# Optimization experiments

Hardware: AMD Instinct MI355X
Metric: run time of the kernel (lower is better)

Reference implementation:

```python
import jax, jax.numpy as jnp
import numpy as np
from jax import lax

# flat indices of the 8 'donut' taps in a 3x3 kernel (center position 4 stays zero),
# matching torch.nonzero row-major ordering of the mask
_DONUT_IDX = jnp.array([0, 1, 2, 3, 5, 6, 7, 8])

def _gelu(x):
    return jax.nn.gelu(x, approximate=False)  # torch nn.GELU default (erf)

def _conv(x, w, dil=1, pad=0):
    return lax.conv_general_dilated(x, w, (1, 1), [(pad, pad), (pad, pad)],
                                    rhs_dilation=(dil, dil),
                                    dimension_numbers=('NCHW', 'OIHW', 'NCHW'))

def _donut_conv(x, p, dil):
    # ParamConv_reg_variable_dilation with shuffle_true=0: scatter 8 params into a
    # 3x3 kernel (zero center) and conv with rhs_dilation=dil, padding=dil ('same').
    O, I, _ = p.shape
    k = jnp.zeros((O, I, 9), p.dtype).at[:, :, _DONUT_IDX].set(p).reshape(O, I, 3, 3)
    return _conv(x, k, dil=dil, pad=dil)

def _resblock(x, w1, w2):
    # gelu(Sequential(conv3x3, gelu, conv3x3)(x) + x)
    return _gelu(_conv(_gelu(_conv(x, w1, pad=1)), w2, pad=1) + x)

def _avgpool2(x):
    N, C, H, W = x.shape
    return x.reshape(N, C, H // 2, 2, W // 2, 2).mean(axis=(3, 5))

def _upsample(x, scale, w):
    # nn.Upsample(scale, bilinear, align_corners=False) -> half-pixel bilinear resize
    N, C, H, W = x.shape
    if scale > 1:
        x = jax.image.resize(x, (N, C, H * scale, W * scale), method='bilinear')
    return _gelu(_conv(x, w))  # 1x1 conv + gelu

def _shine_fwd(input_image, conv0a_w, conv0b_w, first_p, cl10_w, cl2_w,
               dil_p, dilres_p, ups_w, out1_w, out2_w, last_w):
    # n_frames=5, center frame index 2; H,W divisible by 64 so no pad branch
    target = input_image[:, 2:3]
    feats = jnp.concatenate([input_image[:, :2], input_image[:, 3:]], axis=1)  # [N,4,H,W]
    target = _gelu(_conv(target, conv0b_w))            # 1x1 -> 48 ch
    feats = _gelu(_conv(feats, conv0a_w, pad=1))       # 3x3 -> 16 ch
    base = jnp.concatenate([target, feats], axis=1)    # 64 ch

    outs = [_gelu(_donut_conv(base, first_p, 1))]      # first_output (dil 1)
    base = _resblock(base, cl10_w[0, 0], cl10_w[0, 1])
    outs.append(_gelu(_donut_conv(base, dilres_p[0], 3)))  # dilated_convs_res[0]
    base = _resblock(base, cl2_w[0, 0], cl2_w[0, 1])

    dils = (5, 8, 10, 11)     # dilated_convs effective dilations (add_dilation=0)
    dilres = (3, 6, 8, 9)     # dilated_convs_res effective dilations
    for i in range(4):
        m = _gelu(_donut_conv(base, dil_p[i], dils[i]))
        outs.append(_upsample(m, 2 ** i, ups_w[i]))
        if i < 3:
            base = _avgpool2(base)
            base = _resblock(base, cl10_w[i + 1, 0], cl10_w[i + 1, 1])
            m = _gelu(_donut_conv(base, dilres_p[i + 1], dilres[i + 1]))
            outs.append(_upsample(m, 2 ** (i + 1), ups_w[i + 1]))
            base = _resblock(base, cl2_w[i + 1, 0], cl2_w[i + 1, 1])

    out = jnp.concatenate(outs, axis=1)                # 9*64 = 576 ch
    out = _gelu(_conv(out, out1_w))                    # 1x1 576->288
    out = _gelu(_conv(out, out2_w))                    # 1x1 288->64
    return _conv(out, last_w)                          # 1x1 64->1

def setup_inputs():
    key = jax.random.key(0)
    ks = jax.random.split(key, 12)
    s = 0.05
    F = 64
    return {
        'input_image': jax.random.normal(ks[0], (2, 5, 256, 256), jnp.float32),
        'conv0a_w': jax.random.normal(ks[1], (16, 4, 3, 3), jnp.float32) * s,
        'conv0b_w': jax.random.normal(ks[2], (48, 1, 1, 1), jnp.float32) * s,
        'first_p': jax.random.normal(ks[3], (F, F, 8), jnp.float32) * s,
        'cl10_w': jax.random.normal(ks[4], (4, 2, F, F, 3, 3), jnp.float32) * s,
        'cl2_w': jax.random.normal(ks[5], (4, 2, F, F, 3, 3), jnp.float32) * s,
        'dil_p': jax.random.normal(ks[6], (4, F, F, 8), jnp.float32) * s,
        'dilres_p': jax.random.normal(ks[7], (4, F, F, 8), jnp.float32) * s,
        'ups_w': jax.random.normal(ks[8], (4, F, F, 1, 1), jnp.float32) * s,
        'out1_w': jax.random.normal(ks[9], (288, 576, 1, 1), jnp.float32) * s,
        'out2_w': jax.random.normal(ks[10], (64, 288, 1, 1), jnp.float32) * s,
        'last_w': jax.random.normal(ks[11], (1, 64, 1, 1), jnp.float32) * s,
    }

def reference(input_image, conv0a_w, conv0b_w, first_p, cl10_w, cl2_w,
              dil_p, dilres_p, ups_w, out1_w, out2_w, last_w):
    return _shine_fwd(input_image, conv0a_w, conv0b_w, first_p, cl10_w, cl2_w,
                      dil_p, dilres_p, ups_w, out1_w, out2_w, last_w)
```

## Files before the change

### kernel.cpp

```cpp
#include <hip/hip_runtime.h>
#include <hip/hip_bf16.h>


#define HPX 65536
#define FCH 64
#define CHPX 32768

typedef __attribute__((ext_vector_type(8))) short  short8;
typedef __attribute__((ext_vector_type(4))) float  floatx4;

__device__ __forceinline__ float gelu_f(float x) {
  return 0.5f * x * (1.0f + erff(x * 0.70710678118654752440f));
}
__device__ __forceinline__ unsigned short f2bf(float x) {
  unsigned u = __float_as_uint(x);
  unsigned r = (u + 0x7FFFu + ((u >> 16) & 1u)) >> 16;
  return (unsigned short)r;
}
__device__ __forceinline__ float bf2f(unsigned short h) {
  return __uint_as_float(((unsigned)h) << 16);
}

__global__ __launch_bounds__(256) void conv0_nhwc_kernel(
    const float* __restrict__ img,
    const float* __restrict__ w0a,
    const float* __restrict__ w0b,
    unsigned short* __restrict__ ohi,
    unsigned short* __restrict__ olo)
{
  long t = (long)blockIdx.x * 256 + threadIdx.x;
  int c  = (int)(t & 63);
  int px = (int)((t >> 6) & (HPX - 1));
  int n  = (int)(t >> 22);
  const float* im = img + (long)n * 5 * HPX;
  float r;
  if (c < 48) {
    r = w0b[c] * im[2 * HPX + px];
  } else {
    int co = c - 48;
    int y = px >> 8, x = px & 255;
    r = 0.0f;
    const int map4[4] = {0, 1, 3, 4};
    #pragma unroll
    for (int fi = 0; fi < 4; fi++) {
      const float* imc = im + (long)map4[fi] * HPX;
      #pragma unroll
      for (int ky = 0; ky < 3; ky++) {
        int yy = y + ky - 1;
        #pragma unroll
        for (int kx = 0; kx < 3; kx++) {
          int xx = x + kx - 1;
          bool ok = ((unsigned)yy < 256u) && ((unsigned)xx < 256u);
          float v = ok ? imc[yy * 256 + xx] : 0.0f;
          r = fmaf(w0a[((co * 4 + fi) * 3 + ky) * 3 + kx], v, r);
        }
      }
    }
  }
  float v = gelu_f(r);
  unsigned short hb = f2bf(v);
  ohi[t] = hb;
  olo[t] = f2bf(v - bf2f(hb));
}

struct JobArr { int4 j[29]; };

__global__ __launch_bounds__(256) void pack_conv_kernel(
    const float* __restrict__ cl10, const float* __restrict__ cl2,
    const float* __restrict__ first_p, const float* __restrict__ dilres_p,
    const float* __restrict__ dil_p, const float* __restrict__ ups_w,
    unsigned short* __restrict__ packs, JobArr jobs)
{
  int4 jb = jobs.j[blockIdx.y];
  int ntaps = jb.z;
  int idx = blockIdx.x * 256 + threadIdx.x;
  if (idx >= ntaps * 8192) return;
  int j  = idx & 7;
  int l  = (idx >> 3) & 63;
  int s  = (idx >> 9) & 1;
  int nt = (idx >> 10) & 3;
  int kt = (idx >> 12) & 1;
  int tap = idx >> 13;
  int oc = nt * 16 + (l & 15);
  int ci = kt * 32 + (l >> 4) * 8 + j;
  const float* src;
  switch (jb.x) {
    case 0: src = cl10; break;
    case 1: src = cl2; break;
    case 2: src = first_p; break;
    case 3: src = dilres_p; break;
    case 4: src = dil_p; break;
    default: src = ups_w; break;
  }
  float w = src[jb.y + (oc * 64 + ci) * ntaps + tap];
  unsigned short hi = f2bf(w);
  unsigned short v = (s == 0) ? hi : f2bf(w - bf2f(hi));
  packs[jb.w + idx] = v;
}

__global__ __launch_bounds__(256) void pack_w1_kernel(
    const float* __restrict__ w1, unsigned short* __restrict__ w1p)
{
  int t = blockIdx.x * 256 + threadIdx.x;
  if (t >= 18 * 18 * 512) return;
  int j = t & 7, l = (t >> 3) & 63;
  int mt = (t >> 9) % 18, kt = (t >> 9) / 18;
  int oc = mt * 16 + (l & 15);
  int k  = kt * 32 + (l >> 4) * 8 + j;
  float w = w1[oc * 576 + k];
  unsigned short hi = f2bf(w);
  unsigned short lo = f2bf(w - bf2f(hi));
  long base = ((long)(kt * 18 + mt) * 2) * 512 + l * 8 + j;
  w1p[base] = hi;
  w1p[base + 512] = lo;
}
__global__ __launch_bounds__(256) void pack_w2_kernel(
    const float* __restrict__ w2, unsigned short* __restrict__ w2p)
{
  int t = blockIdx.x * 256 + threadIdx.x;
  if (t >= 9 * 4 * 512) return;
  int j = t & 7, l = (t >> 3) & 63;
  int ot = (t >> 9) % 4, kt = (t >> 9) / 4;
  int oc = ot * 16 + (l & 15);
  int k  = kt * 32 + (l >> 4) * 8 + j;
  float w = w2[oc * 288 + k];
  unsigned short hi = f2bf(w);
  unsigned short lo = f2bf(w - bf2f(hi));
  long base = ((long)(kt * 4 + ot) * 2) * 512 + l * 8 + j;
  w2p[base] = hi;
  w2p[base + 512] = lo;
}

template <int NTAPS, int MT, bool RESID, bool TO_CONCAT>
__global__ __launch_bounds__(256) void conv_pipe_kernel(
    const unsigned short* __restrict__ in_hi,
    const unsigned short* __restrict__ in_lo,
    const unsigned short* __restrict__ wp,
    const unsigned short* __restrict__ res_hi,
    const unsigned short* __restrict__ res_lo,
    unsigned short* __restrict__ out_hi,
    unsigned short* __restrict__ out_lo,
    int Hs, int logW, int dil, int ccol)
{
  constexpr int PL = TO_CONCAT ? 1 : 2;
  __shared__ short8 wst[2][1024];
  __shared__ unsigned short tb[4][PL][16][76];
  const int tid  = threadIdx.x;
  const int lane = tid & 63;
  const int wave = tid >> 6;
  const int row  = lane & 15;
  const int g    = lane >> 4;
  const int n    = blockIdx.z;
  const int Ws   = 1 << logW;
  const int npx_in = Hs << logW;
  const int opx0 = blockIdx.x * (64 * MT) + wave * (16 * MT);

  const unsigned short* ihi = in_hi + (long)n * npx_in * 64;
  const unsigned short* ilo = in_lo + (long)n * npx_in * 64;
  const short8* wpv = (const short8*)wp;

  int ry[MT], rx[MT];
  #pragma unroll
  for (int mt = 0; mt < MT; mt++) {
    int p = opx0 + mt * 16 + row;
    ry[mt] = p >> logW;
    rx[mt] = p & (Ws - 1);
  }

  floatx4 acc[MT][4];
  #pragma unroll
  for (int mt = 0; mt < MT; mt++)
    #pragma unroll
    for (int nt = 0; nt < 4; nt++) acc[mt][nt] = (floatx4){0.f, 0.f, 0.f, 0.f};

  const short8 zz = {0, 0, 0, 0, 0, 0, 0, 0};
  short8 sreg[4];
  short8 ahA[MT][2], alA[MT][2], ahB[MT][2], alB[MT][2];

  auto stage_issue = [&](int t) {
    #pragma unroll
    for (int p = 0; p < 4; p++)
      sreg[p] = wpv[(long)t * 1024 + tid + p * 256];
  };
  auto stage_write = [&](int b) {
    #pragma unroll
    for (int p = 0; p < 4; p++)
      wst[b][tid + p * 256] = sreg[p];
  };
  auto a_load = [&](short8 (&ah)[MT][2], short8 (&al)[MT][2], int t) {
    const int kk  = (NTAPS == 9) ? t : (t < 4 ? t : t + 1);
    const int dyd = (kk / 3 - 1) * dil, dxd = (kk % 3 - 1) * dil;
    #pragma unroll
    for (int mt = 0; mt < MT; mt++) {
      int yy = ry[mt] + dyd, xx = rx[mt] + dxd;
      bool ok = ((unsigned)yy < (unsigned)Hs) && ((unsigned)xx < (unsigned)Ws);
      long base = ok ? (long)((yy << logW) + xx) * 64 : 0;
      #pragma unroll
      for (int kt = 0; kt < 2; kt++) {
        long a = base + kt * 32 + g * 8;
        short8 h = *(const short8*)(ihi + a);
        short8 l = *(const short8*)(ilo + a);
        ah[mt][kt] = ok ? h : zz;
        al[mt][kt] = ok ? l : zz;
      }
    }
  };
  auto compute = [&](int b, short8 (&ah)[MT][2], short8 (&al)[MT][2]) {
    #pragma unroll
    for (int kt = 0; kt < 2; kt++)
      #pragma unroll
      for (int nt = 0; nt < 4; nt++) {
        short8 bh = wst[b][(kt * 4 + nt) * 128 + lane];
        short8 bl = wst[b][(kt * 4 + nt) * 128 + 64 + lane];
        #pragma unroll
        for (int mt = 0; mt < MT; mt++) {
          acc[mt][nt] = __builtin_amdgcn_mfma_f32_16x16x32_bf16(ah[mt][kt], bh, acc[mt][nt], 0, 0, 0);
          acc[mt][nt] = __builtin_amdgcn_mfma_f32_16x16x32_bf16(ah[mt][kt], bl, acc[mt][nt], 0, 0, 0);
          acc[mt][nt] = __builtin_amdgcn_mfma_f32_16x16x32_bf16(al[mt][kt], bh, acc[mt][nt], 0, 0, 0);
        }
      }
  };

  stage_issue(0);
  a_load(ahA, alA, 0);
  stage_write(0);
  __syncthreads();

  #pragma unroll
  for (int tt = 0; tt < NTAPS; tt++) {
    const int b = tt & 1;
    if (tt + 1 < NTAPS) {
      stage_issue(tt + 1);
      if ((tt & 1) == 0) a_load(ahB, alB, tt + 1);
      else               a_load(ahA, alA, tt + 1);
    }
    if ((tt & 1) == 0) compute(b, ahA, alA);
    else               compute(b, ahB, alB);
    if (tt + 1 < NTAPS) {
      stage_write(b ^ 1);
      __syncthreads();
    }
  }

  #pragma unroll
  for (int mt = 0; mt < MT; mt++) {
    __builtin_amdgcn_wave_barrier();
    #pragma unroll
    for (int nt = 0; nt < 4; nt++) {
      #pragma unroll
      for (int r = 0; r < 4; r++) {
        int px = opx0 + mt * 16 + g * 4 + r;
        int oc = nt * 16 + row;
        float v = acc[mt][nt][r];
        if (RESID) {
          long ri = ((long)n * npx_in + px) * 64 + oc;
          v += bf2f(res_hi[ri]) + bf2f(res_lo[ri]);
        }
        v = gelu_f(v);
        unsigned short hb = f2bf(v);
        tb[wave][0][g * 4 + r][oc] = hb;
        if (!TO_CONCAT)
          tb[wave][PL - 1][g * 4 + r][oc] = f2bf(v - bf2f(hb));
      }
    }
    __builtin_amdgcn_wave_barrier();
    const int pxb = opx0 + mt * 16;
    const int pxl = lane >> 2;
    #pragma unroll
    for (int pl = 0; pl < PL; pl++) {
      #pragma unroll
      for (int it = 0; it < 2; it++) {
        int ch = (lane & 3) + it * 4;
        short8 v8 = *(const short8*)&tb[wave][pl][pxl][ch * 8];
        if (TO_CONCAT) {
          *(short8*)&out_hi[((long)n * HPX + pxb + pxl) * 576 + ccol + ch * 8] = v8;
        } else {
          unsigned short* dst = pl ? out_lo : out_hi;
          *(short8*)&dst[((long)n * npx_in + pxb + pxl) * 64 + ch * 8] = v8;
        }
      }
    }
  }
}

template <int MT>
__global__ __launch_bounds__(256) void ups_mfma_kernel(
    const unsigned short* __restrict__ in_hi,
    const unsigned short* __restrict__ in_lo,
    const unsigned short* __restrict__ wp,
    unsigned short* __restrict__ outc,
    int Hs, int logW, int ccol)
{
  __shared__ short8 wst[1024];
  __shared__ unsigned short tb[4][16][76];
  const int tid  = threadIdx.x;
  const int lane = threadIdx.x & 63;
  const int wave = threadIdx.x >> 6;
  const int row  = lane & 15;
  const int g    = lane >> 4;
  const int n    = blockIdx.z;
  const int npx_in = Hs << logW;
  const int opx0 = blockIdx.x * (64 * MT) + wave * (16 * MT);

  const unsigned short* ihi = in_hi + (long)n * npx_in * 64;
  const unsigned short* ilo = in_lo + (long)n * npx_in * 64;
  const short8* wpv = (const short8*)wp;

  int b00[MT], b01[MT], b10[MT], b11[MT];
  float bwx[MT], bwy[MT];
  #pragma unroll
  for (int mt = 0; mt < MT; mt++) {
    int p = opx0 + mt * 16 + row;
    int Y = p >> 8, X = p & 255;
    float sc = (float)Hs * (1.0f / 256.0f);
    float fy = ((float)Y + 0.5f) * sc - 0.5f;
    float fx = ((float)X + 0.5f) * sc - 0.5f;
    int y0 = (int)floorf(fy), x0 = (int)floorf(fx);
    bwy[mt] = fy - (float)y0; bwx[mt] = fx - (float)x0;
    int y0c = min(max(y0, 0), Hs - 1), y1c = min(max(y0 + 1, 0), Hs - 1);
    int x0c = min(max(x0, 0), Hs - 1), x1c = min(max(x0 + 1, 0), Hs - 1);
    b00[mt] = (y0c * Hs + x0c) * 64; b01[mt] = (y0c * Hs + x1c) * 64;
    b10[mt] = (y1c * Hs + x0c) * 64; b11[mt] = (y1c * Hs + x1c) * 64;
  }

  floatx4 acc[MT][4];
  #pragma unroll
  for (int mt = 0; mt < MT; mt++)
    #pragma unroll
    for (int nt = 0; nt < 4; nt++) acc[mt][nt] = (floatx4){0.f, 0.f, 0.f, 0.f};

  #pragma unroll
  for (int p = 0; p < 4; p++)
    wst[tid + p * 256] = wpv[tid + p * 256];
  __syncthreads();

  #pragma unroll
  for (int kt = 0; kt < 2; kt++) {
    const int ko = kt * 32 + g * 8;
    short8 ah[MT], al[MT];
    #pragma unroll
    for (int mt = 0; mt < MT; mt++) {
      short8 h00 = *(const short8*)(ihi + b00[mt] + ko);
      short8 l00 = *(const short8*)(ilo + b00[mt] + ko);
      short8 h01 = *(const short8*)(ihi + b01[mt] + ko);
      short8 l01 = *(const short8*)(ilo + b01[mt] + ko);
      short8 h10 = *(const short8*)(ihi + b10[mt] + ko);
      short8 l10 = *(const short8*)(ilo + b10[mt] + ko);
      short8 h11 = *(const short8*)(ihi + b11[mt] + ko);
      short8 l11 = *(const short8*)(ilo + b11[mt] + ko);
      short8 hh, ll;
      #pragma unroll
      for (int j = 0; j < 8; j++) {
        float v00 = bf2f((unsigned short)h00[j]) + bf2f((unsigned short)l00[j]);
        float v01 = bf2f((unsigned short)h01[j]) + bf2f((unsigned short)l01[j]);
        float v10 = bf2f((unsigned short)h10[j]) + bf2f((unsigned short)l10[j]);
        float v11 = bf2f((unsigned short)h11[j]) + bf2f((unsigned short)l11[j]);
        float v0 = v00 + bwx[mt] * (v01 - v00);
        float v1 = v10 + bwx[mt] * (v11 - v10);
        float v  = v0 + bwy[mt] * (v1 - v0);
        unsigned short hb = f2bf(v);
        hh[j] = (short)hb;
        ll[j] = (short)f2bf(v - bf2f(hb));
      }
      ah[mt] = hh; al[mt] = ll;
    }
    #pragma unroll
    for (int nt = 0; nt < 4; nt++) {
      short8 bh = wst[(kt * 4 + nt) * 2 * 64 + lane];
      short8 bl = wst[((kt * 4 + nt) * 2 + 1) * 64 + lane];
      #pragma unroll
      for (int mt = 0; mt < MT; mt++) {
        acc[mt][nt] = __builtin_amdgcn_mfma_f32_16x16x32_bf16(ah[mt], bh, acc[mt][nt], 0, 0, 0);
        acc[mt][nt] = __builtin_amdgcn_mfma_f32_16x16x32_bf16(ah[mt], bl, acc[mt][nt], 0, 0, 0);
        acc[mt][nt] = __builtin_amdgcn_mfma_f32_16x16x32_bf16(al[mt], bh, acc[mt][nt], 0, 0, 0);
      }
    }
  }

  #pragma unroll
  for (int mt = 0; mt < MT; mt++) {
    __builtin_amdgcn_wave_barrier();
    #pragma unroll
    for (int nt = 0; nt < 4; nt++)
      #pragma unroll
      for (int r = 0; r < 4; r++)
        tb[wave][g * 4 + r][nt * 16 + row] = f2bf(gelu_f(acc[mt][nt][r]));
    __builtin_amdgcn_wave_barrier();
    const int pxb = opx0 + mt * 16;
    const int pxl = lane >> 2;
    #pragma unroll
    for (int it = 0; it < 2; it++) {
      int ch = (lane & 3) + it * 4;
      short8 v8 = *(const short8*)&tb[wave][pxl][ch * 8];
      *(short8*)&outc[((long)n * HPX + pxb + pxl) * 576 + ccol + ch * 8] = v8;
    }
  }
}

__global__ __launch_bounds__(256) void avgpool_nhwc_kernel(
    const unsigned short* __restrict__ ihi, const unsigned short* __restrict__ ilo,
    unsigned short* __restrict__ ohi, unsigned short* __restrict__ olo,
    int logWo)
{
  const int lognpo = 2 * logWo;
  long t = (long)blockIdx.x * 256 + threadIdx.x;
  int cg = (int)(t & 7);
  int p  = (int)((t >> 3) & ((1 << lognpo) - 1));
  int n  = (int)(t >> (3 + lognpo));
  int y = p >> logWo, x = p & ((1 << logWo) - 1);
  int Wi = 2 << logWo;
  long ib = ((long)n * (4 << lognpo) + (long)(2 * y) * Wi + 2 * x) * 64 + cg * 8;
  short8 h00 = *(const short8*)(ihi + ib);
  short8 h01 = *(const short8*)(ihi + ib + 64);
  short8 h10 = *(const short8*)(ihi + ib + (long)Wi * 64);
  short8 h11 = *(const short8*)(ihi + ib + (long)Wi * 64 + 64);
  short8 l00 = *(const short8*)(ilo + ib);
  short8 l01 = *(const short8*)(ilo + ib + 64);
  short8 l10 = *(const short8*)(ilo + ib + (long)Wi * 64);
  short8 l11 = *(const short8*)(ilo + ib + (long)Wi * 64 + 64);
  short8 oh, ol;
  #pragma unroll
  for (int j = 0; j < 8; j++) {
    float v = 0.25f * ((bf2f((unsigned short)h00[j]) + bf2f((unsigned short)l00[j])) +
                       (bf2f((unsigned short)h01[j]) + bf2f((unsigned short)l01[j])) +
                       (bf2f((unsigned short)h10[j]) + bf2f((unsigned short)l10[j])) +
                       (bf2f((unsigned short)h11[j]) + bf2f((unsigned short)l11[j])));
    unsigned short hb = f2bf(v);
    oh[j] = (short)hb;
    ol[j] = (short)f2bf(v - bf2f(hb));
  }
  long ob = (((long)n << lognpo) + p) * 64 + cg * 8;
  *(short8*)(ohi + ob) = oh;
  *(short8*)(olo + ob) = ol;
}

__global__ __launch_bounds__(256) void out1_gemm_kernel(
    const unsigned short* __restrict__ v,
    const unsigned short* __restrict__ w1p,
    unsigned short* __restrict__ h,
    int cpx)
{
  __shared__ short8 ws8[2400];
  const int tid  = threadIdx.x;
  const int lane = tid & 63;
  const int wave = tid >> 6;
  const int row  = lane & 15;
  const int g    = lane >> 4;
  const int n    = blockIdx.y;
  const int px0  = cpx + blockIdx.x * 64;
  const int mtb  = (wave < 2) ? wave * 5 : 10 + (wave - 2) * 4;
  const int MTN  = (wave < 2) ? 5 : 4;
  const short8* w1v = (const short8*)w1p;

  floatx4 acc[4][5];
  #pragma unroll
  for (int t = 0; t < 4; t++)
    #pragma unroll
    for (int m = 0; m < 5; m++) acc[t][m] = (floatx4){0.f, 0.f, 0.f, 0.f};

  for (int kt = 0; kt < 18; kt++) {
    __syncthreads();
    #pragma unroll
    for (int p = 0; p < 9; p++)
      ws8[tid + p * 256] = w1v[kt * 2304 + tid + p * 256];
    __syncthreads();

    short8 a[4];
    #pragma unroll
    for (int t = 0; t < 4; t++)
      a[t] = *(const short8*)(v + ((long)n * HPX + px0 + t * 16 + row) * 576 +
                              kt * 32 + g * 8);
    #pragma unroll
    for (int m = 0; m < 5; m++) {
      if (m < MTN) {
        short8 bh = ws8[((mtb + m) * 2 + 0) * 64 + lane];
        short8 bl = ws8[((mtb + m) * 2 + 1) * 64 + lane];
        #pragma unroll
        for (int t = 0; t < 4; t++) {
          acc[t][m] = __builtin_amdgcn_mfma_f32_16x16x32_bf16(a[t], bh, acc[t][m], 0, 0, 0);
          acc[t][m] = __builtin_amdgcn_mfma_f32_16x16x32_bf16(a[t], bl, acc[t][m], 0, 0, 0);
        }
      }
    }
  }

  __syncthreads();
  unsigned short* hs2 = (unsigned short*)ws8;
  #pragma unroll
  for (int m = 0; m < 5; m++) {
    if (m < MTN) {
      #pragma unroll
      for (int t = 0; t < 4; t++)
        #pragma unroll
        for (int r = 0; r < 4; r++)
          hs2[(t * 16 + g * 4 + r) * 300 + (mtb + m) * 16 + row] =
              f2bf(gelu_f(acc[t][m][r]));
    }
  }
  __syncthreads();
  #pragma unroll
  for (int p = 0; p < 9; p++) {
    int li = tid + p * 256;
    int px = li / 36, c16 = li % 36;
    short8 v8 = *(const short8*)&hs2[px * 300 + c16 * 8];
    *(short8*)&h[((long)n * CHPX + (px0 - cpx) + px) * 288 + c16 * 8] = v8;
  }
}

__global__ __launch_bounds__(256) void out2_gemm_kernel(
    const unsigned short* __restrict__ h,
    const unsigned short* __restrict__ w2p,
    const float* __restrict__ w3,
    float* __restrict__ out,
    int cpx)
{
  __shared__ short8 w2s[4608];
  const int tid  = threadIdx.x;
  const int lane = tid & 63;
  const int wave = tid >> 6;
  const int row  = lane & 15;
  const int g    = lane >> 4;
  const int n    = blockIdx.y;
  const int pxc  = blockIdx.x * 256 + wave * 64;
  const short8* w2v = (const short8*)w2p;

  #pragma unroll
  for (int p = 0; p < 18; p++)
    w2s[tid + p * 256] = w2v[tid + p * 256];
  __syncthreads();

  floatx4 acc2[4][4];
  #pragma unroll
  for (int t = 0; t < 4; t++)
    #pragma unroll
    for (int ot = 0; ot < 4; ot++) acc2[t][ot] = (floatx4){0.f, 0.f, 0.f, 0.f};

  for (int kt = 0; kt < 9; kt++) {
    short8 a[4];
    #pragma unroll
    for (int t = 0; t < 4; t++)
      a[t] = *(const short8*)&h[((long)n * CHPX + pxc + t * 16 + row) * 288 +
                                kt * 32 + g * 8];
    #pragma unroll
    for (int ot = 0; ot < 4; ot++) {
      short8 bh = w2s[((kt * 4 + ot) * 2 + 0) * 64 + lane];
      short8 bl = w2s[((kt * 4 + ot) * 2 + 1) * 64 + lane];
      #pragma unroll
      for (int t = 0; t < 4; t++) {
        acc2[t][ot] = __builtin_amdgcn_mfma_f32_16x16x32_bf16(a[t], bh, acc2[t][ot], 0, 0, 0);
        acc2[t][ot] = __builtin_amdgcn_mfma_f32_16x16x32_bf16(a[t], bl, acc2[t][ot], 0, 0, 0);
      }
    }
  }

  float w3r[4];
  #pragma unroll
  for (int ot = 0; ot < 4; ot++) w3r[ot] = w3[ot * 16 + row];
  #pragma unroll
  for (int t = 0; t < 4; t++) {
    float r[4] = {0.f, 0.f, 0.f, 0.f};
    #pragma unroll
    for (int ot = 0; ot < 4; ot++)
      #pragma unroll
      for (int rr = 0; rr < 4; rr++)
        r[rr] = fmaf(w3r[ot], gelu_f(acc2[t][ot][rr]), r[rr]);
    #pragma unroll
    for (int rr = 0; rr < 4; rr++) {
      r[rr] += __shfl_xor(r[rr], 1);
      r[rr] += __shfl_xor(r[rr], 2);
      r[rr] += __shfl_xor(r[rr], 4);
      r[rr] += __shfl_xor(r[rr], 8);
    }
    if (row == 0) {
      int px = cpx + pxc + t * 16 + g * 4;
      #pragma unroll
      for (int rr = 0; rr < 4; rr++)
        out[(long)n * HPX + px + rr] = r[rr];
    }
  }
}

extern "C" void kernel_launch(void* const* d_in, const int* in_sizes, int n_in,
                              void* d_out, int out_size, void* d_ws, size_t ws_size,
                              hipStream_t stream) {
  const float* img      = (const float*)d_in[0];
  const float* w0a      = (const float*)d_in[1];
  const float* w0b      = (const float*)d_in[2];
  const float* first_p  = (const float*)d_in[3];
  const float* cl10     = (const float*)d_in[4];
  const float* cl2      = (const float*)d_in[5];
  const float* dil_p    = (const float*)d_in[6];
  const float* dilres_p = (const float*)d_in[7];
  const float* ups_w    = (const float*)d_in[8];
  const float* w1       = (const float*)d_in[9];
  const float* w2       = (const float*)d_in[10];
  const float* w3       = (const float*)d_in[11];

  const size_t CONCAT_B = 150994944ul;
  const size_t ACT_B    = 16777216ul;
  const size_t PACKS_B  = 3604480ul;
  const size_t W1P_B    = 663552ul;
  const size_t W2P_B    = 73728ul;
  const size_t NEED = CONCAT_B + 4 * ACT_B + PACKS_B + W1P_B + W2P_B;

  if (ws_size < NEED) {
    hipMemsetAsync(d_out, 0, (size_t)out_size * 4, stream);
    return;
  }

  char* wsb = (char*)d_ws;
  unsigned short* concat = (unsigned short*)wsb;
  unsigned short* Xhi = (unsigned short*)(wsb + CONCAT_B);
  unsigned short* Xlo = (unsigned short*)(wsb + CONCAT_B + ACT_B);
  unsigned short* Yhi = (unsigned short*)(wsb + CONCAT_B + 2 * ACT_B);
  unsigned short* Ylo = (unsigned short*)(wsb + CONCAT_B + 3 * ACT_B);
  unsigned short* packs = (unsigned short*)(wsb + CONCAT_B + 4 * ACT_B);
  unsigned short* w1p = (unsigned short*)(wsb + CONCAT_B + 4 * ACT_B + PACKS_B);
  unsigned short* w2p = (unsigned short*)(wsb + CONCAT_B + 4 * ACT_B + PACKS_B + W1P_B);
  unsigned short* hbuf = Xhi;

  auto off_cl10   = [](int c) { return (long)c * 73728; };
  auto off_cl2    = [](int c) { return 589824l + (long)c * 73728; };
  const long OFF_FIRST = 1179648;
  auto off_dilres = [](int k) { return 1245184l + (long)k * 65536; };
  auto off_dil    = [](int k) { return 1507328l + (long)k * 65536; };
  auto off_ups    = [](int k) { return 1769472l + (long)k * 8192; };

  JobArr jobs;
  for (int c = 0; c < 8; c++) jobs.j[c]     = {0, c * 36864, 9, (int)off_cl10(c)};
  for (int c = 0; c < 8; c++) jobs.j[8 + c] = {1, c * 36864, 9, (int)off_cl2(c)};
  jobs.j[16] = {2, 0, 8, (int)OFF_FIRST};
  for (int k = 0; k < 4; k++) jobs.j[17 + k] = {3, k * 32768, 8, (int)off_dilres(k)};
  for (int k = 0; k < 4; k++) jobs.j[21 + k] = {4, k * 32768, 8, (int)off_dil(k)};
  for (int k = 0; k < 4; k++) jobs.j[25 + k] = {5, k * 4096, 1, (int)off_ups(k)};
  pack_conv_kernel<<<dim3(288, 29), 256, 0, stream>>>(
      cl10, cl2, first_p, dilres_p, dil_p, ups_w, packs, jobs);
  pack_w1_kernel<<<(18 * 18 * 512 + 255) / 256, 256, 0, stream>>>(w1, w1p);
  pack_w2_kernel<<<(9 * 4 * 512 + 255) / 256, 256, 0, stream>>>(w2, w2p);

  conv0_nhwc_kernel<<<(2 * HPX * 64) / 256, 256, 0, stream>>>(img, w0a, w0b, Xhi, Xlo);

  auto conv9 = [&](const unsigned short* ih, const unsigned short* il, long wo,
                   unsigned short* oh, unsigned short* ol, int Hs, int logW) {
    int npx = Hs << logW;
    if (npx == HPX)
      conv_pipe_kernel<9, 2, false, false><<<dim3(npx / 128, 1, 2), 256, 0, stream>>>(
          ih, il, packs + wo, nullptr, nullptr, oh, ol, Hs, logW, 1, 0);
    else
      conv_pipe_kernel<9, 1, false, false><<<dim3(npx / 64, 1, 2), 256, 0, stream>>>(
          ih, il, packs + wo, nullptr, nullptr, oh, ol, Hs, logW, 1, 0);
  };
  auto conv9r = [&](const unsigned short* ih, const unsigned short* il, long wo,
                    unsigned short* rh, unsigned short* rl, int Hs, int logW) {
    int npx = Hs << logW;
    if (npx == HPX)
      conv_pipe_kernel<9, 2, true, false><<<dim3(npx / 128, 1, 2), 256, 0, stream>>>(
          ih, il, packs + wo, rh, rl, rh, rl, Hs, logW, 1, 0);
    else
      conv_pipe_kernel<9, 1, true, false><<<dim3(npx / 64, 1, 2), 256, 0, stream>>>(
          ih, il, packs + wo, rh, rl, rh, rl, Hs, logW, 1, 0);
  };
  auto donutC = [&](const unsigned short* ih, const unsigned short* il, long wo,
                    int dil, int ccol) {
    conv_pipe_kernel<8, 2, false, true><<<dim3(512, 1, 2), 256, 0, stream>>>(
        ih, il, packs + wo, nullptr, nullptr, concat, nullptr, 256, 8, dil, ccol);
  };
  auto donutA = [&](const unsigned short* ih, const unsigned short* il, long wo,
                    int dil, unsigned short* oh, unsigned short* ol, int Hs, int logW) {
    int npx = Hs << logW;
    if (npx == HPX)
      conv_pipe_kernel<8, 2, false, false><<<dim3(npx / 128, 1, 2), 256, 0, stream>>>(
          ih, il, packs + wo, nullptr, nullptr, oh, ol, Hs, logW, dil, 0);
    else
      conv_pipe_kernel<8, 1, false, false><<<dim3(npx / 64, 1, 2), 256, 0, stream>>>(
          ih, il, packs + wo, nullptr, nullptr, oh, ol, Hs, logW, dil, 0);
  };
  auto upsC = [&](const unsigned short* ih, const unsigned short* il, long wo,
                  int Hs, int logW, int ccol) {
    ups_mfma_kernel<4><<<dim3(256, 1, 2), 256, 0, stream>>>(
        ih, il, packs + wo, concat, Hs, logW, ccol);
  };
  auto avgp = [&](const unsigned short* ih, const unsigned short* il,
                  unsigned short* oh, unsigned short* ol, int logWo) {
    long total = 2l * (1l << (2 * logWo)) * 8;
    avgpool_nhwc_kernel<<<(int)(total / 256), 256, 0, stream>>>(ih, il, oh, ol, logWo);
  };

  donutC(Xhi, Xlo, OFF_FIRST, 1, 0);
  conv9(Xhi, Xlo, off_cl10(0), Yhi, Ylo, 256, 8);
  conv9r(Yhi, Ylo, off_cl10(1), Xhi, Xlo, 256, 8);
  donutC(Xhi, Xlo, off_dilres(0), 3, 64);
  conv9(Xhi, Xlo, off_cl2(0), Yhi, Ylo, 256, 8);
  conv9r(Yhi, Ylo, off_cl2(1), Xhi, Xlo, 256, 8);

  donutA(Xhi, Xlo, off_dil(0), 5, Yhi, Ylo, 256, 8);
  upsC(Yhi, Ylo, off_ups(0), 256, 8, 128);
  avgp(Xhi, Xlo, Yhi, Ylo, 7);
  conv9(Yhi, Ylo, off_cl10(2), Xhi, Xlo, 128, 7);
  conv9r(Xhi, Xlo, off_cl10(3), Yhi, Ylo, 128, 7);
  donutA(Yhi, Ylo, off_dilres(1), 6, Xhi, Xlo, 128, 7);
  upsC(Xhi, Xlo, off_ups(1), 128, 7, 192);
  conv9(Yhi, Ylo, off_cl2(2), Xhi, Xlo, 128, 7);
  conv9r(Xhi, Xlo, off_cl2(3), Yhi, Ylo, 128, 7);

  donutA(Yhi, Ylo, off_dil(1), 8, Xhi, Xlo, 128, 7);
  upsC(Xhi, Xlo, off_ups(1), 128, 7, 256);
  avgp(Yhi, Ylo, Xhi, Xlo, 6);
  conv9(Xhi, Xlo, off_cl10(4), Yhi, Ylo, 64, 6);
  conv9r(Yhi, Ylo, off_cl10(5), Xhi, Xlo, 64, 6);
  donutA(Xhi, Xlo, off_dilres(2), 8, Yhi, Ylo, 64, 6);
  upsC(Yhi, Ylo, off_ups(2), 64, 6, 320);
  conv9(Xhi, Xlo, off_cl2(4), Yhi, Ylo, 64, 6);
  conv9r(Yhi, Ylo, off_cl2(5), Xhi, Xlo, 64, 6);

  donutA(Xhi, Xlo, off_dil(2), 10, Yhi, Ylo, 64, 6);
  upsC(Yhi, Ylo, off_ups(2), 64, 6, 384);
  avgp(Xhi, Xlo, Yhi, Ylo, 5);
  conv9(Yhi, Ylo, off_cl10(6), Xhi, Xlo, 32, 5);
  conv9r(Xhi, Xlo, off_cl10(7), Yhi, Ylo, 32, 5);
  donutA(Yhi, Ylo, off_dilres(3), 9, Xhi, Xlo, 32, 5);
  upsC(Xhi, Xlo, off_ups(3), 32, 5, 448);
  conv9(Yhi, Ylo, off_cl2(6), Xhi, Xlo, 32, 5);
  conv9r(Xhi, Xlo, off_cl2(7), Yhi, Ylo, 32, 5);

  donutA(Yhi, Ylo, off_dil(3), 11, Xhi, Xlo, 32, 5);
  upsC(Xhi, Xlo, off_ups(3), 32, 5, 512);

  for (int c = 0; c < 2; c++) {
    out1_gemm_kernel<<<dim3(CHPX / 64, 2), 256, 0, stream>>>(
        concat, w1p, hbuf, c * CHPX);
    out2_gemm_kernel<<<dim3(CHPX / 256, 2), 256, 0, stream>>>(
        hbuf, w2p, w3, (float*)d_out, c * CHPX);
  }
}
```

Baseline: 1.090 ms.

## Split conv0 into vectorized kernels and vectorize conv epilogue residual/GELU stores

The first conv is split into two kernels. One computes the 48 1x1-channel outputs, eight channels per thread. The other loads the 36-tap neighbourhood once and reuses it for eight 3x3 output channels, and both write short8 vectors instead of scalar stores. The conv_pipe epilogue now stages raw fp32 accumulators in LDS and does the residual load, GELU and hi/lo bf16 split per 8-channel vector, so residual reads become 16-byte loads instead of scattered 2-byte ones. In exchange, LDS use in the epilogue grows and there is an extra kernel launch.

```diff
diff --git a/kernel.cpp b/kernel.cpp
--- a/kernel.cpp
+++ b/kernel.cpp
@@ -21,46 +21,74 @@
   return __uint_as_float(((unsigned)h) << 16);
 }
 
-__global__ __launch_bounds__(256) void conv0_nhwc_kernel(
+__global__ __launch_bounds__(256) void conv0_elem_kernel(
     const float* __restrict__ img,
-    const float* __restrict__ w0a,
     const float* __restrict__ w0b,
     unsigned short* __restrict__ ohi,
     unsigned short* __restrict__ olo)
 {
-  long t = (long)blockIdx.x * 256 + threadIdx.x;
-  int c  = (int)(t & 63);
-  int px = (int)((t >> 6) & (HPX - 1));
-  int n  = (int)(t >> 22);
+  int t = blockIdx.x * 256 + threadIdx.x;
+  int cg = t % 6;
+  int pn = t / 6;
+  int px = pn & (HPX - 1);
+  int n  = pn >> 16;
+  float x = img[(long)n * 5 * HPX + 2 * HPX + px];
+  short8 oh, ol;
+  #pragma unroll
+  for (int j = 0; j < 8; j++) {
+    int c = cg * 8 + j;
+    float v = gelu_f(w0b[c] * x);
+    unsigned short hb = f2bf(v);
+    oh[j] = (short)hb;
+    ol[j] = (short)f2bf(v - bf2f(hb));
+  }
+  long o = ((long)pn) * 64 + cg * 8;
+  *(short8*)&ohi[o] = oh;
+  *(short8*)&olo[o] = ol;
+}
+
+__global__ __launch_bounds__(256) void conv0_conv_kernel(
+    const float* __restrict__ img,
+    const float* __restrict__ w0a,
+    unsigned short* __restrict__ ohi,
+    unsigned short* __restrict__ olo)
+{
+  int t = blockIdx.x * 256 + threadIdx.x;
+  int cg = t & 1;
+  int pn = t >> 1;
+  int px = pn & (HPX - 1);
+  int n  = pn >> 16;
+  int y = px >> 8, x = px & 255;
   const float* im = img + (long)n * 5 * HPX;
-  float r;
-  if (c < 48) {
-    r = w0b[c] * im[2 * HPX + px];
-  } else {
-    int co = c - 48;
-    int y = px >> 8, x = px & 255;
-    r = 0.0f;
-    const int map4[4] = {0, 1, 3, 4};
-    #pragma unroll
-    for (int fi = 0; fi < 4; fi++) {
-      const float* imc = im + (long)map4[fi] * HPX;
-      #pragma unroll
-      for (int ky = 0; ky < 3; ky++) {
-        int yy = y + ky - 1;
-        #pragma unroll
-        for (int kx = 0; kx < 3; kx++) {
-          int xx = x + kx - 1;
-          bool ok = ((unsigned)yy < 256u) && ((unsigned)xx < 256u);
-          float v = ok ? imc[yy * 256 + xx] : 0.0f;
-          r = fmaf(w0a[((co * 4 + fi) * 3 + ky) * 3 + kx], v, r);
-        }
-      }
-    }
-  }
-  float v = gelu_f(r);
-  unsigned short hb = f2bf(v);
-  ohi[t] = hb;
-  olo[t] = f2bf(v - bf2f(hb));
+  const int map4[4] = {0, 1, 3, 4};
+  float vreg[36];
+  #pragma unroll
+  for (int fi = 0; fi < 4; fi++)
+    #pragma unroll
+    for (int ky = 0; ky < 3; ky++)
+      #pragma unroll
+      for (int kx = 0; kx < 3; kx++) {
+        int yy = y + ky - 1, xx = x + kx - 1;
+        bool ok = ((unsigned)yy < 256u) && ((unsigned)xx < 256u);
+        vreg[(fi * 3 + ky) * 3 + kx] =
+            ok ? im[(long)map4[fi] * HPX + yy * 256 + xx] : 0.0f;
+      }
+  short8 oh, ol;
+  #pragma unroll
+  for (int j = 0; j < 8; j++) {
+    int co = cg * 8 + j;
+    const float* wr = w0a + co * 36;
+    float r = 0.0f;
+    #pragma unroll
+    for (int q = 0; q < 36; q++) r = fmaf(wr[q], vreg[q], r);
+    float v = gelu_f(r);
+    unsigned short hb = f2bf(v);
+    oh[j] = (short)hb;
+    ol[j] = (short)f2bf(v - bf2f(hb));
+  }
+  long o = ((long)pn) * 64 + 48 + cg * 8;
+  *(short8*)&ohi[o] = oh;
+  *(short8*)&olo[o] = ol;
 }
 
 struct JobArr { int4 j[29]; };
@@ -142,9 +170,8 @@
     unsigned short* __restrict__ out_lo,
     int Hs, int logW, int dil, int ccol)
 {
-  constexpr int PL = TO_CONCAT ? 1 : 2;
   __shared__ short8 wst[2][1024];
-  __shared__ unsigned short tb[4][PL][16][76];
+  __shared__ float  ftb[4][16][65];
   const int tid  = threadIdx.x;
   const int lane = tid & 63;
   const int wave = tid >> 6;
@@ -246,38 +273,40 @@
   for (int mt = 0; mt < MT; mt++) {
     __builtin_amdgcn_wave_barrier();
     #pragma unroll
-    for (int nt = 0; nt < 4; nt++) {
-      #pragma unroll
-      for (int r = 0; r < 4; r++) {
-        int px = opx0 + mt * 16 + g * 4 + r;
-        int oc = nt * 16 + row;
-        float v = acc[mt][nt][r];
-        if (RESID) {
-          long ri = ((long)n * npx_in + px) * 64 + oc;
-          v += bf2f(res_hi[ri]) + bf2f(res_lo[ri]);
-        }
-        v = gelu_f(v);
-        unsigned short hb = f2bf(v);
-        tb[wave][0][g * 4 + r][oc] = hb;
-        if (!TO_CONCAT)
-          tb[wave][PL - 1][g * 4 + r][oc] = f2bf(v - bf2f(hb));
-      }
-    }
+    for (int nt = 0; nt < 4; nt++)
+      #pragma unroll
+      for (int r = 0; r < 4; r++)
+        ftb[wave][g * 4 + r][nt * 16 + row] = acc[mt][nt][r];
     __builtin_amdgcn_wave_barrier();
     const int pxb = opx0 + mt * 16;
     const int pxl = lane >> 2;
     #pragma unroll
-    for (int pl = 0; pl < PL; pl++) {
-      #pragma unroll
-      for (int it = 0; it < 2; it++) {
-        int ch = (lane & 3) + it * 4;
-        short8 v8 = *(const short8*)&tb[wave][pl][pxl][ch * 8];
-        if (TO_CONCAT) {
-          *(short8*)&out_hi[((long)n * HPX + pxb + pxl) * 576 + ccol + ch * 8] = v8;
-        } else {
-          unsigned short* dst = pl ? out_lo : out_hi;
-          *(short8*)&dst[((long)n * npx_in + pxb + pxl) * 64 + ch * 8] = v8;
-        }
+    for (int it = 0; it < 2; it++) {
+      const int ch = (lane & 3) + it * 4;
+      float vv[8];
+      #pragma unroll
+      for (int j = 0; j < 8; j++) vv[j] = ftb[wave][pxl][ch * 8 + j];
+      if (RESID) {
+        long rb = ((long)n * npx_in + pxb + pxl) * 64 + ch * 8;
+        short8 rh = *(const short8*)(res_hi + rb);
+        short8 rl = *(const short8*)(res_lo + rb);
+        #pragma unroll
+        for (int j = 0; j < 8; j++)
+          vv[j] += bf2f((unsigned short)rh[j]) + bf2f((unsigned short)rl[j]);
+      }
+      short8 oh8, ol8;
+      #pragma unroll
+      for (int j = 0; j < 8; j++) {
+        float v = gelu_f(vv[j]);
+        unsigned short hb = f2bf(v);
+        oh8[j] = (short)hb;
+        ol8[j] = (short)f2bf(v - bf2f(hb));
+      }
+      if (TO_CONCAT) {
+        *(short8*)&out_hi[((long)n * HPX + pxb + pxl) * 576 + ccol + ch * 8] = oh8;
+      } else {
+        *(short8*)&out_hi[((long)n * npx_in + pxb + pxl) * 64 + ch * 8] = oh8;
+        *(short8*)&out_lo[((long)n * npx_in + pxb + pxl) * 64 + ch * 8] = ol8;
       }
     }
   }
@@ -638,7 +667,8 @@
   pack_w1_kernel<<<(18 * 18 * 512 + 255) / 256, 256, 0, stream>>>(w1, w1p);
   pack_w2_kernel<<<(9 * 4 * 512 + 255) / 256, 256, 0, stream>>>(w2, w2p);
 
-  conv0_nhwc_kernel<<<(2 * HPX * 64) / 256, 256, 0, stream>>>(img, w0a, w0b, Xhi, Xlo);
+  conv0_elem_kernel<<<(2 * HPX * 6) / 256, 256, 0, stream>>>(img, w0b, Xhi, Xlo);
+  conv0_conv_kernel<<<(2 * HPX * 2) / 256, 256, 0, stream>>>(img, w0a, Xhi, Xlo);
 
   auto conv9 = [&](const unsigned short* ih, const unsigned short* il, long wo,
                    unsigned short* oh, unsigned short* ol, int Hs, int logW) {
```

Measured after the change: 972.3 us (median of 3 runs). 10.8% less time.
